# Kernel optimization log

Measured on AMD Instinct MI355X. Metric: run time of the kernel, lower is better.

Reference implementation:

```python
import jax, jax.numpy as jnp
import numpy as np

HEADS = 8
DIM_HEAD = 64
SCALE = DIM_HEAD ** -0.5


def setup_inputs() -> dict:
    key = jax.random.key(0)
    ks = jax.random.split(key, 5)
    B, N, M, D = 8, 1024, 1024, 512
    inner = HEADS * DIM_HEAD  # 512
    return {
        "x": jax.random.normal(ks[0], (B, N, D), dtype=jnp.float32),
        "context": jax.random.normal(ks[1], (B, M, D), dtype=jnp.float32),
        "Wq": jax.random.normal(ks[2], (D, inner), dtype=jnp.float32) * (D ** -0.5),
        "Wkv": jax.random.normal(ks[3], (D, 2 * inner), dtype=jnp.float32) * (D ** -0.5),
        "Wo": jax.random.normal(ks[4], (inner, D), dtype=jnp.float32) * (inner ** -0.5),
        "bo": jnp.zeros((D,), dtype=jnp.float32),
    }


def reference(x, context, Wq, Wkv, Wo, bo):
    B, N, D = x.shape
    M = context.shape[1]
    q = x @ Wq                      # [B, N, inner]
    kv = context @ Wkv              # [B, M, 2*inner]
    k, v = jnp.split(kv, 2, axis=-1)
    # b n (h d) -> b h n d
    split_heads = lambda t: t.reshape(t.shape[0], t.shape[1], HEADS, DIM_HEAD).transpose(0, 2, 1, 3)
    q, k, v = split_heads(q), split_heads(k), split_heads(v)
    dots = jnp.einsum('bhid,bhjd->bhij', q, k) * SCALE  # [B, H, N, M]
    attn = jax.nn.softmax(dots, axis=-1)
    out = jnp.einsum('bhij,bhjd->bhid', attn, v)        # [B, H, N, d]
    out = out.transpose(0, 2, 1, 3).reshape(B, N, HEADS * DIM_HEAD)
    return out @ Wo + bo            # [B, N, D]
```

## Files before the change

kernel.cpp:

```cpp
#include <hip/hip_runtime.h>
#include <stdint.h>

#define LOG2E 1.44269504088896340736f
#define QSCALE (0.125f * LOG2E)

typedef __bf16 bf16x8 __attribute__((ext_vector_type(8)));
typedef float floatx4 __attribute__((ext_vector_type(4)));

__device__ __forceinline__ unsigned short bfbits(float f) {
  __bf16 h = (__bf16)f;
  return __builtin_bit_cast(unsigned short, h);
}

__device__ __forceinline__ float fast_exp2(float x) {
#if __has_builtin(__builtin_amdgcn_exp2f)
  return __builtin_amdgcn_exp2f(x);
#else
  return exp2f(x);
#endif
}

__device__ __forceinline__ void gl2lds16(const void* g, void* l) {
  __builtin_amdgcn_global_load_lds((const __attribute__((address_space(1))) void*)g,
                                   (__attribute__((address_space(3))) void*)l, 16, 0, 0);
}

__global__ __launch_bounds__(256)
void prep_kernel(const float* __restrict__ x, const float* __restrict__ ctx,
                 const float* __restrict__ Wq, const float* __restrict__ Wkv,
                 const float* __restrict__ Wo,
                 unsigned short* __restrict__ Xb, unsigned short* __restrict__ Cb,
                 unsigned short* __restrict__ WqT, unsigned short* __restrict__ WkvT,
                 unsigned short* __restrict__ WoT) {
  int blk = blockIdx.x;
  int tid = threadIdx.x;
  if (blk < 8192) {
    const float* in = blk < 4096 ? x : ctx;
    unsigned short* out = blk < 4096 ? Xb : Cb;
    int i = (((blk & 4095) * 256) + tid) * 4;
    float4 v = *(const float4*)(in + i);
    unsigned long long pk = (unsigned long long)bfbits(v.x)
                          | ((unsigned long long)bfbits(v.y) << 16)
                          | ((unsigned long long)bfbits(v.z) << 32)
                          | ((unsigned long long)bfbits(v.w) << 48);
    *(unsigned long long*)(out + i) = pk;
  } else {
    __shared__ float tile[32][33];
    int t = blk - 8192;
    const float* in; unsigned short* out; int N; int tb;
    if (t < 256)      { in = Wq;  out = WqT;  N = 512;  tb = t; }
    else if (t < 768) { in = Wkv; out = WkvT; N = 1024; tb = t - 256; }
    else              { in = Wo;  out = WoT;  N = 512;  tb = t - 768; }
    const int K = 512;
    int nbx = N / 32;
    int n0 = (tb % nbx) * 32, k0 = (tb / nbx) * 32;
    int tx = tid & 31, ty = tid >> 5;
#pragma unroll
    for (int r = ty; r < 32; r += 8)
      tile[r][tx] = in[(long)(k0 + r) * N + n0 + tx];
    __syncthreads();
#pragma unroll
    for (int r = ty; r < 32; r += 8)
      out[(long)(n0 + r) * K + k0 + tx] = bfbits(tile[tx][r]);
  }
}

__global__ __launch_bounds__(256)
void proj_gemm(const unsigned short* __restrict__ Xb, const unsigned short* __restrict__ Cb,
               const unsigned short* __restrict__ WqT, const unsigned short* __restrict__ WkvT,
               unsigned short* __restrict__ Qb, unsigned short* __restrict__ Kb,
               unsigned short* __restrict__ Vt) {
  __shared__ unsigned short As[128 * 64];
  __shared__ unsigned short Bs[128 * 64];

  int idx0 = blockIdx.x;
  int idx = (idx0 & 7) * 96 + (idx0 >> 3);
  const unsigned short* A; const unsigned short* Bt;
  long bm, bn; int role;
  if (idx < 256) { role = 0; A = Xb; Bt = WqT;  bn = (long)(idx & 3) * 128; bm = (long)(idx >> 2) * 128; }
  else { int j = idx - 256; role = 1; A = Cb; Bt = WkvT; bn = (long)(j & 7) * 128; bm = (long)(j >> 3) * 128; }

  const int tid = threadIdx.x;
  const int wave = tid >> 6;
  const int lane = tid & 63;
  const int l15 = lane & 15;
  const int q4 = lane >> 4;
  const int s7 = l15 & 7;
  const int wm = (wave & 1) * 64;
  const int wn = (wave >> 1) * 64;
  const int K = 512;

  int aoff[4], boff[4], lds16[4];
#pragma unroll
  for (int cc = 0; cc < 4; ++cc) {
    int c = cc * 256 + tid;
    int r = c >> 3, kc = c & 7;
    int sw = (kc ^ (r & 7)) * 8;
    aoff[cc] = (int)(bm + r) * K + sw;
    boff[cc] = (int)(bn + r) * K + sw;
    lds16[cc] = c * 16;
  }
  int arow[4], brow[4], csw[2];
#pragma unroll
  for (int i = 0; i < 4; ++i) {
    arow[i] = (wm + i * 16 + l15) * 64;
    brow[i] = (wn + i * 16 + l15) * 64;
  }
#pragma unroll
  for (int ks = 0; ks < 2; ++ks) csw[ks] = ((ks * 4 + q4) ^ s7) * 8;

  floatx4 acc[4][4];
#pragma unroll
  for (int i = 0; i < 4; ++i)
#pragma unroll
    for (int j = 0; j < 4; ++j) { acc[i][j][0]=0.f; acc[i][j][1]=0.f; acc[i][j][2]=0.f; acc[i][j][3]=0.f; }

  for (int k0 = 0; k0 < K; k0 += 64) {
#pragma unroll
    for (int cc = 0; cc < 4; ++cc) {
      gl2lds16(A + aoff[cc] + k0, (char*)As + lds16[cc]);
      gl2lds16(Bt + boff[cc] + k0, (char*)Bs + lds16[cc]);
    }
    __syncthreads();
#pragma unroll
    for (int ks = 0; ks < 2; ++ks) {
      bf16x8 af[4], bfr[4];
#pragma unroll
      for (int i = 0; i < 4; ++i) af[i] = *(const bf16x8*)(As + arow[i] + csw[ks]);
#pragma unroll
      for (int j = 0; j < 4; ++j) bfr[j] = *(const bf16x8*)(Bs + brow[j] + csw[ks]);
#pragma unroll
      for (int i = 0; i < 4; ++i)
#pragma unroll
        for (int j = 0; j < 4; ++j)
          acc[i][j] = __builtin_amdgcn_mfma_f32_16x16x32_bf16(af[i], bfr[j], acc[i][j], 0, 0, 0);
    }
    __syncthreads();
  }

  const bool vrole = (role == 1) && (bn >= 512);
#pragma unroll
  for (int i = 0; i < 4; ++i) {
#pragma unroll
    for (int j = 0; j < 4; ++j) {
      long col = bn + wn + j * 16 + l15;
      if (vrole) {
        long h = (col - 512) >> 6, d = col & 63;
        long row0 = bm + wm + i * 16 + q4 * 4;
        long b = row0 >> 10, m0 = row0 & 1023;
        unsigned long long pk = (unsigned long long)bfbits(acc[i][j][0])
                              | ((unsigned long long)bfbits(acc[i][j][1]) << 16)
                              | ((unsigned long long)bfbits(acc[i][j][2]) << 32)
                              | ((unsigned long long)bfbits(acc[i][j][3]) << 48);
        *(unsigned long long*)(Vt + ((b * 8 + h) * 64 + d) * 1024 + m0) = pk;
      } else {
        long h = col >> 6, d = col & 63;
#pragma unroll
        for (int r = 0; r < 4; ++r) {
          long row = bm + wm + i * 16 + q4 * 4 + r;
          long b = row >> 10, n = row & 1023;
          float v = acc[i][j][r];
          if (role == 0) Qb[((b * 8 + h) * 1024 + n) * 64 + d] = bfbits(v * QSCALE);
          else           Kb[((b * 8 + h) * 1024 + n) * 64 + d] = bfbits(v);
        }
      }
    }
  }
}

__global__ __launch_bounds__(512)
void attn_kernel(const unsigned short* __restrict__ Qb,
                 const unsigned short* __restrict__ Kb,
                 const unsigned short* __restrict__ Vt,
                 unsigned short* __restrict__ Ob)
{
  __shared__ unsigned short Ksm[2][4096];
  __shared__ unsigned short Vsm[2][4096];
  __shared__ unsigned short Psm[128 * 64];

  const int tid = threadIdx.x;
  const int wave = tid >> 6;
  const int lane = tid & 63;
  const int l15 = lane & 15;
  const int q4 = lane >> 4;
  const int bid = blockIdx.x;
  const int lin = (bid & 7) * 64 + (bid >> 3);
  const int bh = lin >> 3;
  const int nb = lin & 7;

  const long qrow0 = (long)bh * 1024 + nb * 128 + wave * 16;

  bf16x8 qf[2];
#pragma unroll
  for (int ks = 0; ks < 2; ++ks)
    qf[ks] = *(const bf16x8*)(Qb + (qrow0 + l15) * 64 + ks * 32 + q4 * 8);

  floatx4 acc[4];
#pragma unroll
  for (int d = 0; d < 4; ++d) { acc[d][0]=0.f; acc[d][1]=0.f; acc[d][2]=0.f; acc[d][3]=0.f; }
  float suml = 0.0f;

  const unsigned short* Kbase = Kb + (long)bh * 65536;
  const unsigned short* Vbase = Vt + (long)bh * 65536;
  const int jrow = tid >> 3;
  const int cact = (tid & 7) ^ (jrow & 7);
  const int koff = jrow * 64 + cact * 8;
  const int voff = jrow * 1024 + cact * 8;
  const int myl = tid * 16;

  const int s7 = l15 & 7;
  int kfo[2][4];
  int pao[2];
  int pwo[4];
#pragma unroll
  for (int ks = 0; ks < 2; ++ks) {
#pragma unroll
    for (int jn = 0; jn < 4; ++jn)
      kfo[ks][jn] = (jn * 16 + l15) * 64 + (((ks * 4 + q4) ^ s7) * 8);
    pao[ks] = (wave * 16 + l15) * 64 + (((ks * 4 + q4) ^ s7) * 8);
  }
#pragma unroll
  for (int jn = 0; jn < 4; ++jn)
    pwo[jn] = (wave * 16 + l15) * 64 + (((jn * 2 + (q4 >> 1)) ^ s7) * 8) + (q4 & 1) * 4;

  gl2lds16(Kbase + koff, (char*)Ksm[0] + myl);
  gl2lds16(Vbase + voff, (char*)Vsm[0] + myl);

#define ATTN_TILE(TIDX, CUR, STAGE)                                                          \
  {                                                                                          \
    __syncthreads();                                                                         \
    if (STAGE) {                                                                             \
      gl2lds16(Kbase + ((TIDX) + 1) * 4096 + koff, (char*)Ksm[(CUR) ^ 1] + myl);             \
      gl2lds16(Vbase + ((TIDX) + 1) * 64 + voff, (char*)Vsm[(CUR) ^ 1] + myl);               \
    }                                                                                        \
    floatx4 st[4];                                                                           \
    _Pragma("unroll")                                                                        \
    for (int jn = 0; jn < 4; ++jn) {                                                         \
      st[jn][0] = 0.f; st[jn][1] = 0.f; st[jn][2] = 0.f; st[jn][3] = 0.f;                    \
    }                                                                                        \
    _Pragma("unroll")                                                                        \
    for (int ks = 0; ks < 2; ++ks) {                                                         \
      bf16x8 kfr[4];                                                                         \
      _Pragma("unroll")                                                                      \
      for (int jn = 0; jn < 4; ++jn)                                                         \
        kfr[jn] = *(const bf16x8*)(Ksm[(CUR)] + kfo[ks][jn]);                                \
      __builtin_amdgcn_s_setprio(1);                                                         \
      _Pragma("unroll")                                                                      \
      for (int jn = 0; jn < 4; ++jn)                                                         \
        st[jn] = __builtin_amdgcn_mfma_f32_16x16x32_bf16(kfr[jn], qf[ks], st[jn], 0, 0, 0);  \
      __builtin_amdgcn_s_setprio(0);                                                         \
    }                                                                                        \
    bf16x8 vbt[2][4];        \
    _Pragma("unroll")                                                                        \
    for (int ks = 0; ks < 2; ++ks)                                                           \
      _Pragma("unroll")                                                                      \
      for (int dn = 0; dn < 4; ++dn)                                                         \
        vbt[ks][dn] = *(const bf16x8*)(Vsm[(CUR)] + kfo[ks][dn]);                            \
    _Pragma("unroll")                                                                        \
    for (int jn = 0; jn < 4; ++jn) {                                                         \
      float p0 = fast_exp2(st[jn][0]);                                                       \
      float p1 = fast_exp2(st[jn][1]);                                                       \
      float p2 = fast_exp2(st[jn][2]);                                                       \
      float p3 = fast_exp2(st[jn][3]);                                                       \
      suml += (p0 + p1) + (p2 + p3);                                                         \
      unsigned int lo = (unsigned int)bfbits(p0) | ((unsigned int)bfbits(p1) << 16);         \
      unsigned int hi = (unsigned int)bfbits(p2) | ((unsigned int)bfbits(p3) << 16);         \
      unsigned long long pk = (unsigned long long)lo | ((unsigned long long)hi << 32);       \
      *(unsigned long long*)(Psm + pwo[jn]) = pk;                                            \
    }                                                                                        \
    __asm__ volatile("s_waitcnt lgkmcnt(0)" ::: "memory");                                   \
    _Pragma("unroll")                                                                        \
    for (int ks = 0; ks < 2; ++ks) {                                                         \
      bf16x8 pa = *(const bf16x8*)(Psm + pao[ks]);                                           \
      __builtin_amdgcn_s_setprio(1);                                                         \
      _Pragma("unroll")                                                                      \
      for (int dn = 0; dn < 4; ++dn)                                                         \
        acc[dn] = __builtin_amdgcn_mfma_f32_16x16x32_bf16(pa, vbt[ks][dn], acc[dn], 0, 0, 0);\
      __builtin_amdgcn_s_setprio(0);                                                         \
    }                                                                                        \
  }

  for (int tt = 0; tt < 8; ++tt) {
    ATTN_TILE(2 * tt, 0, true);
    ATTN_TILE(2 * tt + 1, 1, (tt < 7));
  }
#undef ATTN_TILE

  float l = suml;
  l += __shfl_xor(l, 16, 64);
  l += __shfl_xor(l, 32, 64);
  float inv = 1.0f / l;
  float invr[4];
#pragma unroll
  for (int r = 0; r < 4; ++r) invr[r] = __shfl(inv, q4 * 4 + r, 64);

  const int b = bh >> 3, h = bh & 7;
#pragma unroll
  for (int dn = 0; dn < 4; ++dn) {
#pragma unroll
    for (int r = 0; r < 4; ++r) {
      long row = (long)b * 1024 + nb * 128 + wave * 16 + q4 * 4 + r;
      long col = h * 64 + dn * 16 + l15;
      Ob[row * 512 + col] = bfbits(acc[dn][r] * invr[r]);
    }
  }
}

__global__ __launch_bounds__(256)
void out_gemm(const unsigned short* __restrict__ A,
              const unsigned short* __restrict__ Bt,
              float* __restrict__ outF, const float* __restrict__ bias) {
  __shared__ unsigned short As[64 * 64];
  __shared__ unsigned short Bs[64 * 64];

  int bid = blockIdx.x;
  int swz = (bid & 7) * 128 + (bid >> 3);
  const long bm = (long)(swz >> 3) * 64;
  const long bn = (long)(swz & 7) * 64;

  const int tid = threadIdx.x;
  const int wave = tid >> 6;
  const int lane = tid & 63;
  const int l15 = lane & 15;
  const int q4 = lane >> 4;
  const int s7 = l15 & 7;
  const int wm = (wave & 1) * 32;
  const int wn = (wave >> 1) * 32;
  const int K = 512, N = 512;

  int aoff[2], boff[2], lds16[2];
#pragma unroll
  for (int cc = 0; cc < 2; ++cc) {
    int c = cc * 256 + tid;
    int r = c >> 3, kc = c & 7;
    int sw = (kc ^ (r & 7)) * 8;
    aoff[cc] = (int)(bm + r) * K + sw;
    boff[cc] = (int)(bn + r) * K + sw;
    lds16[cc] = c * 16;
  }
  int arow[2], brow[2], csw[2];
#pragma unroll
  for (int i = 0; i < 2; ++i) {
    arow[i] = (wm + i * 16 + l15) * 64;
    brow[i] = (wn + i * 16 + l15) * 64;
  }
#pragma unroll
  for (int ks = 0; ks < 2; ++ks) csw[ks] = ((ks * 4 + q4) ^ s7) * 8;

  floatx4 acc[2][2];
#pragma unroll
  for (int i = 0; i < 2; ++i)
#pragma unroll
    for (int j = 0; j < 2; ++j) { acc[i][j][0]=0.f; acc[i][j][1]=0.f; acc[i][j][2]=0.f; acc[i][j][3]=0.f; }

  for (int k0 = 0; k0 < K; k0 += 64) {
#pragma unroll
    for (int cc = 0; cc < 2; ++cc) {
      gl2lds16(A + aoff[cc] + k0, (char*)As + lds16[cc]);
      gl2lds16(Bt + boff[cc] + k0, (char*)Bs + lds16[cc]);
    }
    __syncthreads();
#pragma unroll
    for (int ks = 0; ks < 2; ++ks) {
      bf16x8 af[2], bfr[2];
#pragma unroll
      for (int i = 0; i < 2; ++i) af[i] = *(const bf16x8*)(As + arow[i] + csw[ks]);
#pragma unroll
      for (int j = 0; j < 2; ++j) bfr[j] = *(const bf16x8*)(Bs + brow[j] + csw[ks]);
#pragma unroll
      for (int i = 0; i < 2; ++i)
#pragma unroll
        for (int j = 0; j < 2; ++j)
          acc[i][j] = __builtin_amdgcn_mfma_f32_16x16x32_bf16(af[i], bfr[j], acc[i][j], 0, 0, 0);
    }
    __syncthreads();
  }

#pragma unroll
  for (int i = 0; i < 2; ++i) {
#pragma unroll
    for (int j = 0; j < 2; ++j) {
      long col = bn + wn + j * 16 + l15;
      float bv = bias[col];
#pragma unroll
      for (int r = 0; r < 4; ++r) {
        long row = bm + wm + i * 16 + q4 * 4 + r;
        outF[row * (long)N + col] = acc[i][j][r] + bv;
      }
    }
  }
}

extern "C" void kernel_launch(void* const* d_in, const int* in_sizes, int n_in,
                              void* d_out, int out_size, void* d_ws, size_t ws_size,
                              hipStream_t stream) {
  const float* x   = (const float*)d_in[0];
  const float* ctx = (const float*)d_in[1];
  const float* Wq  = (const float*)d_in[2];
  const float* Wkv = (const float*)d_in[3];
  const float* Wo  = (const float*)d_in[4];
  const float* bo  = (const float*)d_in[5];
  float* out = (float*)d_out;

  char* ws = (char*)d_ws;
  unsigned short* Xb   = (unsigned short*)(ws);
  unsigned short* Cb   = (unsigned short*)(ws + (8u  << 20));
  unsigned short* WqT  = (unsigned short*)(ws + (16u << 20));
  unsigned short* WkvT = (unsigned short*)(ws + (17u << 20));
  unsigned short* WoT  = (unsigned short*)(ws + (19u << 20));
  unsigned short* Qb   = (unsigned short*)(ws + (20u << 20));
  unsigned short* Kb   = (unsigned short*)(ws + (28u << 20));
  unsigned short* Vt   = (unsigned short*)(ws + (36u << 20));
  unsigned short* Ob   = (unsigned short*)(ws + (44u << 20));

  prep_kernel<<<9216, 256, 0, stream>>>(x, ctx, Wq, Wkv, Wo, Xb, Cb, WqT, WkvT, WoT);
  proj_gemm<<<768, 256, 0, stream>>>(Xb, Cb, WqT, WkvT, Qb, Kb, Vt);
  attn_kernel<<<512, 512, 0, stream>>>(Qb, Kb, Vt, Ob);
  out_gemm<<<1024, 256, 0, stream>>>(Ob, WoT, out, bo);
}
```

Measured before the change: 150.7 us.

## Double-buffer LDS tiles with BK=32 in projection and output GEMMs

Both the QKV projection GEMM and the output GEMM switch from a single 64-wide K tile to two 32-wide LDS buffers. The global-to-LDS load for the next K step is issued before the MFMAs on the current buffer, so each step needs one barrier instead of two. The intent is to overlap global memory latency with matrix math. The LDS swizzle is rewritten for the 32-wide rows. The cost is twice as many K iterations and barriers. There is also no explicit wait on the async LDS loads beyond __syncthreads.

```diff
diff --git a/kernel.cpp b/kernel.cpp
--- a/kernel.cpp
+++ b/kernel.cpp
@@ -70,8 +70,8 @@
                const unsigned short* __restrict__ WqT, const unsigned short* __restrict__ WkvT,
                unsigned short* __restrict__ Qb, unsigned short* __restrict__ Kb,
                unsigned short* __restrict__ Vt) {
-  __shared__ unsigned short As[128 * 64];
-  __shared__ unsigned short Bs[128 * 64];
+  __shared__ unsigned short As[2][128 * 32];
+  __shared__ unsigned short Bs[2][128 * 32];
 
   int idx0 = blockIdx.x;
   int idx = (idx0 & 7) * 96 + (idx0 >> 3);
@@ -85,29 +85,27 @@
   const int lane = tid & 63;
   const int l15 = lane & 15;
   const int q4 = lane >> 4;
-  const int s7 = l15 & 7;
   const int wm = (wave & 1) * 64;
   const int wn = (wave >> 1) * 64;
   const int K = 512;
 
-  int aoff[4], boff[4], lds16[4];
-#pragma unroll
-  for (int cc = 0; cc < 4; ++cc) {
+  int aoff[2], boff[2], lds16[2];
+#pragma unroll
+  for (int cc = 0; cc < 2; ++cc) {
     int c = cc * 256 + tid;
-    int r = c >> 3, kc = c & 7;
-    int sw = (kc ^ (r & 7)) * 8;
-    aoff[cc] = (int)(bm + r) * K + sw;
-    boff[cc] = (int)(bn + r) * K + sw;
+    int r = c >> 2, kc = c & 3;
+    int gc = kc ^ ((r >> 1) & 3);
+    aoff[cc] = (int)(bm + r) * K + gc * 8;
+    boff[cc] = (int)(bn + r) * K + gc * 8;
     lds16[cc] = c * 16;
   }
-  int arow[4], brow[4], csw[2];
+  const int csw = (q4 ^ ((l15 >> 1) & 3)) * 8;
+  int arow[4], brow[4];
 #pragma unroll
   for (int i = 0; i < 4; ++i) {
-    arow[i] = (wm + i * 16 + l15) * 64;
-    brow[i] = (wn + i * 16 + l15) * 64;
-  }
-#pragma unroll
-  for (int ks = 0; ks < 2; ++ks) csw[ks] = ((ks * 4 + q4) ^ s7) * 8;
+    arow[i] = (wm + i * 16 + l15) * 32 + csw;
+    brow[i] = (wn + i * 16 + l15) * 32 + csw;
+  }
 
   floatx4 acc[4][4];
 #pragma unroll
@@ -115,28 +113,39 @@
 #pragma unroll
     for (int j = 0; j < 4; ++j) { acc[i][j][0]=0.f; acc[i][j][1]=0.f; acc[i][j][2]=0.f; acc[i][j][3]=0.f; }
 
-  for (int k0 = 0; k0 < K; k0 += 64) {
-#pragma unroll
-    for (int cc = 0; cc < 4; ++cc) {
-      gl2lds16(A + aoff[cc] + k0, (char*)As + lds16[cc]);
-      gl2lds16(Bt + boff[cc] + k0, (char*)Bs + lds16[cc]);
-    }
-    __syncthreads();
-#pragma unroll
-    for (int ks = 0; ks < 2; ++ks) {
-      bf16x8 af[4], bfr[4];
-#pragma unroll
-      for (int i = 0; i < 4; ++i) af[i] = *(const bf16x8*)(As + arow[i] + csw[ks]);
-#pragma unroll
-      for (int j = 0; j < 4; ++j) bfr[j] = *(const bf16x8*)(Bs + brow[j] + csw[ks]);
-#pragma unroll
-      for (int i = 0; i < 4; ++i)
-#pragma unroll
-        for (int j = 0; j < 4; ++j)
-          acc[i][j] = __builtin_amdgcn_mfma_f32_16x16x32_bf16(af[i], bfr[j], acc[i][j], 0, 0, 0);
-    }
-    __syncthreads();
-  }
+#define PROJ_STAGE(BUF, KOFF)                                              \
+  {                                                                        \
+    _Pragma("unroll")                                                      \
+    for (int cc = 0; cc < 2; ++cc) {                                       \
+      gl2lds16(A + aoff[cc] + (KOFF), (char*)As[(BUF)] + lds16[cc]);       \
+      gl2lds16(Bt + boff[cc] + (KOFF), (char*)Bs[(BUF)] + lds16[cc]);      \
+    }                                                                      \
+  }
+
+#define PROJ_STEP(T, CUR, DO_STAGE)                                        \
+  {                                                                        \
+    if (DO_STAGE) PROJ_STAGE((CUR) ^ 1, ((T) + 1) * 32);                   \
+    bf16x8 af[4], bfr[4];                                                  \
+    _Pragma("unroll")                                                      \
+    for (int i = 0; i < 4; ++i) af[i] = *(const bf16x8*)(As[(CUR)] + arow[i]); \
+    _Pragma("unroll")                                                      \
+    for (int j = 0; j < 4; ++j) bfr[j] = *(const bf16x8*)(Bs[(CUR)] + brow[j]); \
+    _Pragma("unroll")                                                      \
+    for (int i = 0; i < 4; ++i)                                            \
+      _Pragma("unroll")                                                    \
+      for (int j = 0; j < 4; ++j)                                          \
+        acc[i][j] = __builtin_amdgcn_mfma_f32_16x16x32_bf16(af[i], bfr[j], acc[i][j], 0, 0, 0); \
+    if ((T) < 15) __syncthreads();                                         \
+  }
+
+  PROJ_STAGE(0, 0);
+  __syncthreads();
+  for (int tt = 0; tt < 8; ++tt) {
+    PROJ_STEP(2 * tt, 0, true);
+    PROJ_STEP(2 * tt + 1, 1, (tt < 7));
+  }
+#undef PROJ_STEP
+#undef PROJ_STAGE
 
   const bool vrole = (role == 1) && (bn >= 512);
 #pragma unroll
@@ -310,8 +319,8 @@
 void out_gemm(const unsigned short* __restrict__ A,
               const unsigned short* __restrict__ Bt,
               float* __restrict__ outF, const float* __restrict__ bias) {
-  __shared__ unsigned short As[64 * 64];
-  __shared__ unsigned short Bs[64 * 64];
+  __shared__ unsigned short As[2][64 * 32];
+  __shared__ unsigned short Bs[2][64 * 32];
 
   int bid = blockIdx.x;
   int swz = (bid & 7) * 128 + (bid >> 3);
@@ -323,29 +332,23 @@
   const int lane = tid & 63;
   const int l15 = lane & 15;
   const int q4 = lane >> 4;
-  const int s7 = l15 & 7;
   const int wm = (wave & 1) * 32;
   const int wn = (wave >> 1) * 32;
   const int K = 512, N = 512;
 
-  int aoff[2], boff[2], lds16[2];
-#pragma unroll
-  for (int cc = 0; cc < 2; ++cc) {
-    int c = cc * 256 + tid;
-    int r = c >> 3, kc = c & 7;
-    int sw = (kc ^ (r & 7)) * 8;
-    aoff[cc] = (int)(bm + r) * K + sw;
-    boff[cc] = (int)(bn + r) * K + sw;
-    lds16[cc] = c * 16;
-  }
-  int arow[2], brow[2], csw[2];
+  const int r = tid >> 2, kc = tid & 3;
+  const int gc = kc ^ ((r >> 1) & 3);
+  const int aoff = (int)(bm + r) * K + gc * 8;
+  const int boff = (int)(bn + r) * K + gc * 8;
+  const int myl = tid * 16;
+
+  const int csw = (q4 ^ ((l15 >> 1) & 3)) * 8;
+  int arow[2], brow[2];
 #pragma unroll
   for (int i = 0; i < 2; ++i) {
-    arow[i] = (wm + i * 16 + l15) * 64;
-    brow[i] = (wn + i * 16 + l15) * 64;
-  }
-#pragma unroll
-  for (int ks = 0; ks < 2; ++ks) csw[ks] = ((ks * 4 + q4) ^ s7) * 8;
+    arow[i] = (wm + i * 16 + l15) * 32 + csw;
+    brow[i] = (wn + i * 16 + l15) * 32 + csw;
+  }
 
   floatx4 acc[2][2];
 #pragma unroll
@@ -353,28 +356,36 @@
 #pragma unroll
     for (int j = 0; j < 2; ++j) { acc[i][j][0]=0.f; acc[i][j][1]=0.f; acc[i][j][2]=0.f; acc[i][j][3]=0.f; }
 
-  for (int k0 = 0; k0 < K; k0 += 64) {
-#pragma unroll
-    for (int cc = 0; cc < 2; ++cc) {
-      gl2lds16(A + aoff[cc] + k0, (char*)As + lds16[cc]);
-      gl2lds16(Bt + boff[cc] + k0, (char*)Bs + lds16[cc]);
-    }
-    __syncthreads();
-#pragma unroll
-    for (int ks = 0; ks < 2; ++ks) {
-      bf16x8 af[2], bfr[2];
-#pragma unroll
-      for (int i = 0; i < 2; ++i) af[i] = *(const bf16x8*)(As + arow[i] + csw[ks]);
-#pragma unroll
-      for (int j = 0; j < 2; ++j) bfr[j] = *(const bf16x8*)(Bs + brow[j] + csw[ks]);
-#pragma unroll
-      for (int i = 0; i < 2; ++i)
-#pragma unroll
-        for (int j = 0; j < 2; ++j)
-          acc[i][j] = __builtin_amdgcn_mfma_f32_16x16x32_bf16(af[i], bfr[j], acc[i][j], 0, 0, 0);
-    }
-    __syncthreads();
-  }
+#define OUT_STAGE(BUF, KOFF)                                        \
+  {                                                                 \
+    gl2lds16(A + aoff + (KOFF), (char*)As[(BUF)] + myl);            \
+    gl2lds16(Bt + boff + (KOFF), (char*)Bs[(BUF)] + myl);           \
+  }
+
+#define OUT_STEP(T, CUR, DO_STAGE)                                  \
+  {                                                                 \
+    if (DO_STAGE) OUT_STAGE((CUR) ^ 1, ((T) + 1) * 32);             \
+    bf16x8 af[2], bfr[2];                                           \
+    _Pragma("unroll")                                               \
+    for (int i = 0; i < 2; ++i) af[i] = *(const bf16x8*)(As[(CUR)] + arow[i]); \
+    _Pragma("unroll")                                               \
+    for (int j = 0; j < 2; ++j) bfr[j] = *(const bf16x8*)(Bs[(CUR)] + brow[j]); \
+    _Pragma("unroll")                                               \
+    for (int i = 0; i < 2; ++i)                                     \
+      _Pragma("unroll")                                             \
+      for (int j = 0; j < 2; ++j)                                   \
+        acc[i][j] = __builtin_amdgcn_mfma_f32_16x16x32_bf16(af[i], bfr[j], acc[i][j], 0, 0, 0); \
+    if ((T) < 15) __syncthreads();                                  \
+  }
+
+  OUT_STAGE(0, 0);
+  __syncthreads();
+  for (int tt = 0; tt < 8; ++tt) {
+    OUT_STEP(2 * tt, 0, true);
+    OUT_STEP(2 * tt + 1, 1, (tt < 7));
+  }
+#undef OUT_STEP
+#undef OUT_STAGE
 
 #pragma unroll
   for (int i = 0; i < 2; ++i) {
@@ -383,9 +394,9 @@
       long col = bn + wn + j * 16 + l15;
       float bv = bias[col];
 #pragma unroll
-      for (int r = 0; r < 4; ++r) {
-        long row = bm + wm + i * 16 + q4 * 4 + r;
-        outF[row * (long)N + col] = acc[i][j][r] + bv;
+      for (int rr = 0; rr < 4; ++rr) {
+        long row = bm + wm + i * 16 + q4 * 4 + rr;
+        outF[row * (long)N + col] = acc[i][j][rr] + bv;
       }
     }
   }
```

Result: slower. 158.1 us (+4.9%).
